# Optimization experiments

Measured on AMD Instinct MI355X. Metric: run time of the kernel, lower is better.

## Reference

```python
import jax, jax.numpy as jnp
import numpy as np

N, E, F_IN, F_HID, F_OUT = 50000, 800000, 128, 128, 64


def setup_inputs() -> dict:
    key = jax.random.key(0)
    k_x, k_e, k_w1, k_w2 = jax.random.split(key, 4)
    x = jax.random.normal(k_x, (N, F_IN), dtype=jnp.float32)
    edge_index = jax.random.randint(k_e, (2, E), 0, N, dtype=jnp.int32)
    # GCNConv params (glorot-ish scale)
    W1 = jax.random.normal(k_w1, (F_IN, F_HID), dtype=jnp.float32) * (1.0 / np.sqrt(F_IN))
    b1 = jnp.zeros((F_HID,), dtype=jnp.float32)
    W2 = jax.random.normal(k_w2, (F_HID, F_OUT), dtype=jnp.float32) * (1.0 / np.sqrt(F_HID))
    b2 = jnp.zeros((F_OUT,), dtype=jnp.float32)
    return {"x": x, "edge_index": edge_index, "W1": W1, "b1": b1, "W2": W2, "b2": b2}


def reference(x, edge_index, W1, b1, W2, b2):
    n = x.shape[0]
    # PyG GCNConv: add self-loops, symmetric normalization deg^-1/2 * deg^-1/2
    loops = jnp.arange(n, dtype=edge_index.dtype)
    src = jnp.concatenate([edge_index[0], loops])  # (E+N,)
    dst = jnp.concatenate([edge_index[1], loops])  # (E+N,)
    deg = jax.ops.segment_sum(jnp.ones_like(dst, dtype=x.dtype), dst, num_segments=n)
    dinv = jnp.where(deg > 0, jax.lax.rsqrt(jnp.maximum(deg, 1.0)), 0.0)
    norm = dinv[src] * dinv[dst]  # (E+N,)

    def conv(h, W, b):
        h = h @ W                               # (n, f_out)
        msg = h[src] * norm[:, None]            # gather + scale, (E+N, f_out)
        return jax.ops.segment_sum(msg, dst, num_segments=n) + b

    h = jax.nn.relu(conv(x, W1, b1))  # dropout p=0.0 -> identity
    return conv(h, W2, b2)
```

## Files before the change

kernel.cpp:

```cpp
#include <hip/hip_runtime.h>

typedef __bf16 bf16x8 __attribute__((ext_vector_type(8)));
typedef float  f32x4  __attribute__((ext_vector_type(4)));
typedef int    i32x4  __attribute__((ext_vector_type(4)));
typedef unsigned int u32x4 __attribute__((ext_vector_type(4)));

#define NTLOAD(p)    __builtin_nontemporal_load(p)

__device__ __forceinline__ float bf2f(unsigned short h) {
    return __uint_as_float(((unsigned int)h) << 16);
}
__device__ __forceinline__ unsigned short f2bf(float f) {
    unsigned int u = __float_as_uint(f);
    u += 0x7FFFu + ((u >> 16) & 1u);
    return (unsigned short)(u >> 16);
}
__device__ __forceinline__ void unpack8(u32x4 u, float* v) {
#pragma unroll
    for (int k = 0; k < 4; ++k) {
        v[2 * k]     = __uint_as_float(u[k] << 16);
        v[2 * k + 1] = __uint_as_float(u[k] & 0xFFFF0000u);
    }
}

__global__ void k1_deg_detect(const int* __restrict__ dst, int* __restrict__ deg,
                              int* __restrict__ rank, int E,
                              const unsigned short* __restrict__ x, int* __restrict__ cnt,
                              int degBlocks) {
    if ((int)blockIdx.x < degBlocks) {
        int e0 = (blockIdx.x * 256 + threadIdx.x) * 8;
        if (e0 + 8 <= E) {
            i32x4 d0 = NTLOAD((i32x4*)(dst + e0));
            i32x4 d1 = NTLOAD((i32x4*)(dst + e0 + 4));
            i32x4 r0, r1;
#pragma unroll
            for (int k = 0; k < 4; ++k) r0[k] = atomicAdd(&deg[d0[k]], 1);
#pragma unroll
            for (int k = 0; k < 4; ++k) r1[k] = atomicAdd(&deg[d1[k]], 1);
            *(i32x4*)(rank + e0)     = r0;
            *(i32x4*)(rank + e0 + 4) = r1;
        } else {
            for (int e = e0; e < E; ++e) rank[e] = atomicAdd(&deg[dst[e]], 1);
        }
    } else {
        int c = 0;
        for (int i = threadIdx.x; i < 4096; i += 256) {
            unsigned e = (x[i] >> 7) & 0xFFu;
            if (e >= 0x88u) ++c;
        }
        if (c) atomicAdd(cnt, c);
    }
}

template <int COLS>
__device__ __forceinline__ void prepack_one(const void* W, unsigned short* Wp, int idx,
                                            bool isf32) {
    if (idx >= (COLS / 16) * 4 * 64) return;
    int lane = idx & 63;
    int ks   = (idx >> 6) & 3;
    int nt   = idx >> 8;
    int col  = nt * 16 + (lane & 15);
    int krow = ks * 32 + (lane >> 4) * 8;
    unsigned short tmp[8];
#pragma unroll
    for (int j = 0; j < 8; ++j) {
        size_t e = (size_t)(krow + j) * COLS + col;
        float v = isf32 ? ((const float*)W)[e] : bf2f(((const unsigned short*)W)[e]);
        tmp[j] = f2bf(v);
    }
    *(u32x4*)(Wp + (size_t)idx * 8) = *(u32x4*)tmp;
}

__global__ void k2_scan1_prep(const int* __restrict__ deg, int* __restrict__ offs,
                              int* __restrict__ bsum, float* __restrict__ dinv, int N, int NB,
                              const void* __restrict__ W1, const void* __restrict__ W2,
                              const void* __restrict__ b1, const void* __restrict__ b2,
                              unsigned short* __restrict__ Wp1, unsigned short* __restrict__ Wp2,
                              float* __restrict__ b1f, float* __restrict__ b2f,
                              const int* __restrict__ cnt) {
    __shared__ int s[256];
    int t = threadIdx.x;
    if ((int)blockIdx.x < NB) {
        int base = blockIdx.x * 1024 + t * 4;
        int d4[4];
#pragma unroll
        for (int k = 0; k < 4; ++k) d4[k] = (base + k < N) ? deg[base + k] : 0;
#pragma unroll
        for (int k = 0; k < 4; ++k)
            if (base + k < N) dinv[base + k] = rsqrtf((float)d4[k] + 1.0f);
        int mySum = d4[0] + d4[1] + d4[2] + d4[3];
        s[t] = mySum;
        __syncthreads();
        for (int d = 1; d < 256; d <<= 1) {
            int v = (t >= d) ? s[t - d] : 0;
            __syncthreads();
            s[t] += v;
            __syncthreads();
        }
        int run = s[t] - mySum;
#pragma unroll
        for (int k = 0; k < 4; ++k) {
            if (base + k < N) offs[base + k] = run;
            run += d4[k];
        }
        if (t == 255) bsum[blockIdx.x] = s[255];
    } else {
        bool isf32 = (*cnt >= 16);
        int bid = blockIdx.x - NB;
        if (bid < 8) {
            prepack_one<128>(W1, Wp1, bid * 256 + t, isf32);
        } else if (bid < 12) {
            prepack_one<64>(W2, Wp2, (bid - 8) * 256 + t, isf32);
        } else {
            if (t < 128) b1f[t] = isf32 ? ((const float*)b1)[t]
                                        : bf2f(((const unsigned short*)b1)[t]);
            else if (t < 192) b2f[t - 128] = isf32 ? ((const float*)b2)[t - 128]
                                                   : bf2f(((const unsigned short*)b2)[t - 128]);
        }
    }
}

__global__ void scan23(const int* __restrict__ bsum, int* __restrict__ offs,
                       int N, int E, int NB) {
    __shared__ int s[256];
    int t = threadIdx.x;
    s[t] = (t < NB) ? bsum[t] : 0;
    __syncthreads();
    for (int d = 1; d < 256; d <<= 1) {
        int v = (t >= d) ? s[t - d] : 0;
        __syncthreads();
        s[t] += v;
        __syncthreads();
    }
    int boff = (blockIdx.x > 0) ? s[blockIdx.x - 1] : 0;
    int base = blockIdx.x * 1024 + t * 4;
#pragma unroll
    for (int k = 0; k < 4; ++k) {
        int i = base + k;
        if (i < N) offs[i] += boff;
    }
    if (blockIdx.x == 0 && t == 0) offs[N] = E;
}

__device__ __forceinline__ void gemm1_body(const void* __restrict__ X,
                                           const unsigned short* __restrict__ Wp,
                                           const float* __restrict__ dinv,
                                           unsigned short* __restrict__ O, int nstrips,
                                           bool xf32, int blockI) {
    constexpr int NT = 8;
    const int wave = threadIdx.x >> 6;
    const int lane = threadIdx.x & 63;
    const int strip = blockI * 4 + wave;
    if (strip >= nstrips) return;
    const int m = lane & 15;
    const int q = lane >> 4;
    const unsigned rowoff = (unsigned)(strip * 16 + m) * 128u + (unsigned)(q * 8);

    f32x4 acc[NT];
#pragma unroll
    for (int nt = 0; nt < NT; ++nt) acc[nt] = (f32x4){0.f, 0.f, 0.f, 0.f};

#pragma unroll
    for (int ks = 0; ks < 4; ++ks) {
        bf16x8 a;
        if (xf32) {
            const float* xp = (const float*)X + rowoff + ks * 32;
            f32x4 u = NTLOAD((f32x4*)xp);
            f32x4 v = NTLOAD((f32x4*)xp + 1);
            unsigned short tmp[8];
            tmp[0] = f2bf(u[0]); tmp[1] = f2bf(u[1]); tmp[2] = f2bf(u[2]); tmp[3] = f2bf(u[3]);
            tmp[4] = f2bf(v[0]); tmp[5] = f2bf(v[1]); tmp[6] = f2bf(v[2]); tmp[7] = f2bf(v[3]);
            a = *(bf16x8*)tmp;
        } else {
            a = NTLOAD((bf16x8*)((const unsigned short*)X + rowoff + ks * 32));
        }
#pragma unroll
        for (int nt = 0; nt < NT; ++nt) {
            bf16x8 b = *(const bf16x8*)(Wp + (unsigned)(((nt * 4 + ks) * 64 + lane) * 8));
            acc[nt] = __builtin_amdgcn_mfma_f32_16x16x32_bf16(a, b, acc[nt], 0, 0, 0);
        }
    }

    const int r0 = strip * 16 + q * 4;
    f32x4 dv = *(const f32x4*)(dinv + r0);
    float dr[4] = {dv[0], dv[1], dv[2], dv[3]};
#pragma unroll
    for (int nt = 0; nt < NT; ++nt) {
#pragma unroll
        for (int r = 0; r < 4; ++r)
            O[(unsigned)(r0 + r) * 128u + (unsigned)(nt * 16 + m)] = f2bf(acc[nt][r] * dr[r]);
    }
}

__global__ __launch_bounds__(256) void k5_scatter_gemm1(
        const int* __restrict__ src, const int* __restrict__ dst,
        const int* __restrict__ offs, const int* __restrict__ rank,
        int* __restrict__ adj, int E, int SB,
        const void* __restrict__ X, const unsigned short* __restrict__ Wp,
        const float* __restrict__ dinv,
        unsigned short* __restrict__ O, int nstrips, const int* __restrict__ cnt) {
    if ((int)blockIdx.x < SB) {
        int e0 = (blockIdx.x * 256 + threadIdx.x) * 8;
        if (e0 + 8 <= E) {
            i32x4 d0 = NTLOAD((i32x4*)(dst + e0));
            i32x4 d1 = NTLOAD((i32x4*)(dst + e0 + 4));
            i32x4 s0 = NTLOAD((i32x4*)(src + e0));
            i32x4 s1 = NTLOAD((i32x4*)(src + e0 + 4));
            i32x4 r0 = NTLOAD((i32x4*)(rank + e0));
            i32x4 r1 = NTLOAD((i32x4*)(rank + e0 + 4));
            adj[offs[d0[0]] + r0[0]] = s0[0];
            adj[offs[d0[1]] + r0[1]] = s0[1];
            adj[offs[d0[2]] + r0[2]] = s0[2];
            adj[offs[d0[3]] + r0[3]] = s0[3];
            adj[offs[d1[0]] + r1[0]] = s1[0];
            adj[offs[d1[1]] + r1[1]] = s1[1];
            adj[offs[d1[2]] + r1[2]] = s1[2];
            adj[offs[d1[3]] + r1[3]] = s1[3];
        } else {
            for (int e = e0; e < E; ++e) adj[offs[dst[e]] + rank[e]] = src[e];
        }
    } else {
        gemm1_body(X, Wp, dinv, O, nstrips, (*cnt >= 16), blockIdx.x - SB);
    }
}

__global__ __launch_bounds__(256) void gather1_gemm2(
        const unsigned short* __restrict__ Hb, const float* __restrict__ dinv,
        const float* __restrict__ b, const int* __restrict__ offs,
        const int* __restrict__ adj, const unsigned short* __restrict__ Wp2,
        unsigned short* __restrict__ H2b, int N) {
    __shared__ unsigned short Rs[16][136];
    const int strip = blockIdx.x;
    const int lane = threadIdx.x & 63;

    {
        int ndl = threadIdx.x >> 4;
        int nd = strip * 16 + ndl;
        int l15 = lane & 15;
        int gbase = lane & ~15;
        unsigned f8 = (unsigned)(l15 * 8);
        if (nd < N) {
            float acc[8];
#pragma unroll
            for (int k = 0; k < 8; ++k) acc[k] = 0.f;
            int beg = offs[nd], end = offs[nd + 1];
            for (int c = beg; c < end; c += 16) {
                int rem = end - c;
                int myadj = (l15 < rem) ? NTLOAD((int*)&adj[c + l15]) : 0;
#pragma unroll
                for (int t = 0; t < 16; t += 8) {
                    if (t >= rem) break;
                    int sI[8];
#pragma unroll
                    for (int k = 0; k < 8; ++k) sI[k] = __shfl(myadj, gbase + t + k, 64);
                    u32x4 u[8];
#pragma unroll
                    for (int k = 0; k < 8; ++k)
                        u[k] = *(const u32x4*)(Hb + ((unsigned)sI[k] << 7) + f8);
                    float n[8];
#pragma unroll
                    for (int k = 0; k < 8; ++k) n[k] = (t + k < rem) ? 1.f : 0.f;
#pragma unroll
                    for (int k = 0; k < 8; ++k) {
                        float v[8];
                        unpack8(u[k], v);
#pragma unroll
                        for (int j = 0; j < 8; ++j) acc[j] = fmaf(v[j], n[k], acc[j]);
                    }
                }
            }
            float dd = dinv[nd];
            float hv[8], bb[8];
            unpack8(*(const u32x4*)(Hb + ((unsigned)nd << 7) + f8), hv);
            *(f32x4*)&bb[0] = *(const f32x4*)(b + f8);
            *(f32x4*)&bb[4] = *(const f32x4*)(b + f8 + 4);
            unsigned short o[8];
#pragma unroll
            for (int k = 0; k < 8; ++k) {
                float a = fmaf(acc[k] + hv[k], dd, bb[k]);
                o[k] = f2bf(fmaxf(a, 0.f));
            }
            *(u32x4*)&Rs[ndl][f8] = *(u32x4*)o;
        } else {
            *(u32x4*)&Rs[ndl][f8] = (u32x4){0u, 0u, 0u, 0u};
        }
    }
    __syncthreads();

    {
        const int nt = threadIdx.x >> 6;
        const int m = lane & 15;
        const int q = lane >> 4;
        f32x4 acc = (f32x4){0.f, 0.f, 0.f, 0.f};
#pragma unroll
        for (int ks = 0; ks < 4; ++ks) {
            bf16x8 a = *(const bf16x8*)&Rs[m][ks * 32 + q * 8];
            bf16x8 bfr = *(const bf16x8*)(Wp2 + (unsigned)(((nt * 4 + ks) * 64 + lane) * 8));
            acc = __builtin_amdgcn_mfma_f32_16x16x32_bf16(a, bfr, acc, 0, 0, 0);
        }
        const int r0 = strip * 16 + q * 4;
        if (r0 + 3 < N) {
            f32x4 dv = *(const f32x4*)(dinv + r0);
#pragma unroll
            for (int r = 0; r < 4; ++r)
                H2b[(unsigned)(r0 + r) * 64u + (unsigned)(nt * 16 + m)] = f2bf(acc[r] * dv[r]);
        } else {
#pragma unroll
            for (int r = 0; r < 4; ++r) {
                int row = r0 + r;
                if (row < N)
                    H2b[(unsigned)row * 64u + (unsigned)(nt * 16 + m)] =
                        f2bf(acc[r] * dinv[row]);
            }
        }
    }
}

__global__ void gather2(const unsigned short* __restrict__ H2b, const float* __restrict__ dinv,
                        const float* __restrict__ b, const int* __restrict__ offs,
                        const int* __restrict__ adj, void* __restrict__ out,
                        int N, const int* __restrict__ cnt) {
    bool isf32 = (*cnt >= 16);
    int nd = blockIdx.x * 32 + (threadIdx.x >> 3);
    int lane = threadIdx.x & 63;
    int l7 = lane & 7;
    int gbase = lane & ~7;
    unsigned f8 = (unsigned)(l7 * 8);
    if (nd >= N) return;

    float acc[8];
#pragma unroll
    for (int k = 0; k < 8; ++k) acc[k] = 0.f;

    int beg = offs[nd], end = offs[nd + 1];
    for (int c = beg; c < end; c += 8) {
        int rem = end - c;
        int myadj = (l7 < rem) ? NTLOAD((int*)&adj[c + l7]) : 0;
        int sI[8];
#pragma unroll
        for (int k = 0; k < 8; ++k) sI[k] = __shfl(myadj, gbase + k, 64);
        u32x4 u[8];
#pragma unroll
        for (int k = 0; k < 8; ++k)
            u[k] = *(const u32x4*)(H2b + ((unsigned)sI[k] << 6) + f8);
        float n[8];
#pragma unroll
        for (int k = 0; k < 8; ++k) n[k] = (k < rem) ? 1.f : 0.f;
#pragma unroll
        for (int k = 0; k < 8; ++k) {
            float v[8];
            unpack8(u[k], v);
#pragma unroll
            for (int j = 0; j < 8; ++j) acc[j] = fmaf(v[j], n[k], acc[j]);
        }
    }
    float dd = dinv[nd];
    float hv[8], bb[8];
    unpack8(*(const u32x4*)(H2b + ((unsigned)nd << 6) + f8), hv);
    *(f32x4*)&bb[0] = *(const f32x4*)(b + f8);
    *(f32x4*)&bb[4] = *(const f32x4*)(b + f8 + 4);
    float r[8];
#pragma unroll
    for (int k = 0; k < 8; ++k) r[k] = fmaf(acc[k] + hv[k], dd, bb[k]);
    if (isf32) {
        float* op = (float*)out + (unsigned)nd * 64u + f8;
        *(f32x4*)op       = *(f32x4*)&r[0];
        *(f32x4*)(op + 4) = *(f32x4*)&r[4];
    } else {
        unsigned short o[8];
#pragma unroll
        for (int k = 0; k < 8; ++k) o[k] = f2bf(r[k]);
        *(u32x4*)((unsigned short*)out + (unsigned)nd * 64u + f8) = *(u32x4*)o;
    }
}

extern "C" void kernel_launch(void* const* d_in, const int* in_sizes, int n_in,
                              void* d_out, int out_size, void* d_ws, size_t ws_size,
                              hipStream_t stream) {
    const void* x  = d_in[0];
    const int*  ei = (const int*)d_in[1];
    const void* W1 = d_in[2];
    const void* b1 = d_in[3];
    const void* W2 = d_in[4];
    const void* b2 = d_in[5];

    const int N = in_sizes[0] / 128;
    const int E = in_sizes[1] / 2;
    const int* src = ei;
    const int* dst = ei + E;

    float* ws = (float*)d_ws;
    size_t off = 0;
    auto alloc = [&](size_t n) { size_t p = off; off += (n + 15) & ~(size_t)15; return p; };
    int*   cnt    = (int*)(ws + alloc(64));
    int*   deg    = (int*)(ws + alloc(N));
    float* dinv   = ws + alloc(N);
    int*   offs   = (int*)(ws + alloc(N + 1));
    int*   bsum   = (int*)(ws + alloc(256));
    int*   adj    = (int*)(ws + alloc(E));
    int*   rank   = (int*)(ws + alloc(E));
    unsigned short* Hb  = (unsigned short*)(ws + alloc((size_t)N * 64));
    unsigned short* Wp1 = (unsigned short*)(ws + alloc(8192));
    unsigned short* Wp2 = (unsigned short*)(ws + alloc(4096));
    float* b1f    = ws + alloc(128);
    float* b2f    = ws + alloc(64);
    unsigned short* H2b = (unsigned short*)(ws + alloc((size_t)N * 32));

    hipMemsetAsync(ws, 0, (64 + ((size_t)(N + 15) & ~(size_t)15)) * sizeof(float), stream);

    const int EB8 = (E + 2047) / 2048;
    const int NB = (N + 1023) / 1024;
    const int nstrips = (N + 15) / 16;
    const int GB = (nstrips + 3) / 4;

    k1_deg_detect<<<EB8 + 1, 256, 0, stream>>>(dst, deg, rank, E,
                                               (const unsigned short*)x, cnt, EB8);
    k2_scan1_prep<<<NB + 13, 256, 0, stream>>>(deg, offs, bsum, dinv, N, NB,
                                               W1, W2, b1, b2, Wp1, Wp2, b1f, b2f, cnt);
    scan23<<<NB, 256, 0, stream>>>(bsum, offs, N, E, NB);
    k5_scatter_gemm1<<<EB8 + GB, 256, 0, stream>>>(src, dst, offs, rank, adj, E, EB8,
                                                   x, Wp1, dinv, Hb, nstrips, cnt);
    gather1_gemm2<<<nstrips, 256, 0, stream>>>(Hb, dinv, b1f, offs, adj, Wp2, H2b, N);
    gather2<<<(N + 31) / 32, 256, 0, stream>>>(H2b, dinv, b2f, offs, adj, d_out, N, cnt);
}
```

Before: 191.2 us.

## Double-buffer neighbor gathers and double threads per node in both gather kernels

Both gather kernels now assign twice as many threads per destination node, each loading 8-byte slices instead of 16-byte slices. The neighbor loop is software-pipelined with two register buffers, so the next 8 neighbor rows are issued before the current 8 are accumulated. Adjacency indices are fetched in 32-wide windows and refreshed as needed. The aim is more memory-level parallelism and better latency hiding on the random row gathers. The cost is more threads and narrower loads, and gather1_gemm2 now uses 512-thread blocks with half the threads idle during the MFMA phase.

```diff
diff --git a/kernel.cpp b/kernel.cpp
--- a/kernel.cpp
+++ b/kernel.cpp
@@ -14,13 +14,6 @@
     unsigned int u = __float_as_uint(f);
     u += 0x7FFFu + ((u >> 16) & 1u);
     return (unsigned short)(u >> 16);
-}
-__device__ __forceinline__ void unpack8(u32x4 u, float* v) {
-#pragma unroll
-    for (int k = 0; k < 4; ++k) {
-        v[2 * k]     = __uint_as_float(u[k] << 16);
-        v[2 * k + 1] = __uint_as_float(u[k] & 0xFFFF0000u);
-    }
 }
 
 __global__ void k1_deg_detect(const int* __restrict__ dst, int* __restrict__ deg,
@@ -224,71 +217,94 @@
     }
 }
 
-__global__ __launch_bounds__(256) void gather1_gemm2(
+__global__ __launch_bounds__(512) void gather1_gemm2(
         const unsigned short* __restrict__ Hb, const float* __restrict__ dinv,
         const float* __restrict__ b, const int* __restrict__ offs,
         const int* __restrict__ adj, const unsigned short* __restrict__ Wp2,
         unsigned short* __restrict__ H2b, int N) {
     __shared__ unsigned short Rs[16][136];
     const int strip = blockIdx.x;
-    const int lane = threadIdx.x & 63;
+    const int tid = threadIdx.x;
+    const int lane = tid & 63;
 
     {
-        int ndl = threadIdx.x >> 4;
+        int ndl = tid >> 5;
         int nd = strip * 16 + ndl;
-        int l15 = lane & 15;
-        int gbase = lane & ~15;
-        unsigned f8 = (unsigned)(l15 * 8);
+        int l31 = tid & 31;
+        int gbase = lane & ~31;
+        unsigned fb = (unsigned)(l31 * 4);
         if (nd < N) {
-            float acc[8];
-#pragma unroll
-            for (int k = 0; k < 8; ++k) acc[k] = 0.f;
             int beg = offs[nd], end = offs[nd + 1];
-            for (int c = beg; c < end; c += 16) {
-                int rem = end - c;
-                int myadj = (l15 < rem) ? NTLOAD((int*)&adj[c + l15]) : 0;
-#pragma unroll
-                for (int t = 0; t < 16; t += 8) {
-                    if (t >= rem) break;
-                    int sI[8];
-#pragma unroll
-                    for (int k = 0; k < 8; ++k) sI[k] = __shfl(myadj, gbase + t + k, 64);
-                    u32x4 u[8];
-#pragma unroll
-                    for (int k = 0; k < 8; ++k)
-                        u[k] = *(const u32x4*)(Hb + ((unsigned)sI[k] << 7) + f8);
-                    float n[8];
-#pragma unroll
-                    for (int k = 0; k < 8; ++k) n[k] = (t + k < rem) ? 1.f : 0.f;
-#pragma unroll
-                    for (int k = 0; k < 8; ++k) {
-                        float v[8];
-                        unpack8(u[k], v);
-#pragma unroll
-                        for (int j = 0; j < 8; ++j) acc[j] = fmaf(v[j], n[k], acc[j]);
-                    }
+            int wbase = beg;
+            int ma = (wbase + l31 < end) ? adj[wbase + l31] : 0;
+            uint2 self = *(const uint2*)(Hb + ((unsigned)nd << 7) + fb);
+            float dd = dinv[nd];
+            f32x4 bb = *(const f32x4*)(b + fb);
+
+            float acc[4] = {0.f, 0.f, 0.f, 0.f};
+            uint2 ua[8], ub[8];
+
+            auto issue8 = [&](uint2* u, int c0) {
+                int off = c0 - wbase;
+#pragma unroll
+                for (int k = 0; k < 8; ++k) {
+                    int s = __shfl(ma, gbase + off + k, 64);
+                    u[k] = *(const uint2*)(Hb + ((unsigned)s << 7) + fb);
                 }
+            };
+            auto consume8 = [&](const uint2* u, int c0) {
+#pragma unroll
+                for (int k = 0; k < 8; ++k) {
+                    float w = (c0 + k < end) ? 1.f : 0.f;
+                    acc[0] = fmaf(__uint_as_float(u[k].x << 16), w, acc[0]);
+                    acc[1] = fmaf(__uint_as_float(u[k].x & 0xFFFF0000u), w, acc[1]);
+                    acc[2] = fmaf(__uint_as_float(u[k].y << 16), w, acc[2]);
+                    acc[3] = fmaf(__uint_as_float(u[k].y & 0xFFFF0000u), w, acc[3]);
+                }
+            };
+            auto refresh = [&](int c0) {
+                if (c0 - wbase >= 32) {
+                    wbase = c0;
+                    ma = (wbase + l31 < end) ? adj[wbase + l31] : 0;
+                }
+            };
+
+            int cA = beg;
+            issue8(ua, cA);
+            for (;;) {
+                int cB = cA + 8;
+                if (cB < end) {
+                    refresh(cB);
+                    issue8(ub, cB);
+                    consume8(ua, cA);
+                    int cN = cB + 8;
+                    if (cN < end) {
+                        refresh(cN);
+                        issue8(ua, cN);
+                        consume8(ub, cB);
+                        cA = cN;
+                    } else { consume8(ub, cB); break; }
+                } else { consume8(ua, cA); break; }
             }
-            float dd = dinv[nd];
-            float hv[8], bb[8];
-            unpack8(*(const u32x4*)(Hb + ((unsigned)nd << 7) + f8), hv);
-            *(f32x4*)&bb[0] = *(const f32x4*)(b + f8);
-            *(f32x4*)&bb[4] = *(const f32x4*)(b + f8 + 4);
-            unsigned short o[8];
-#pragma unroll
-            for (int k = 0; k < 8; ++k) {
-                float a = fmaf(acc[k] + hv[k], dd, bb[k]);
-                o[k] = f2bf(fmaxf(a, 0.f));
-            }
-            *(u32x4*)&Rs[ndl][f8] = *(u32x4*)o;
-        } else {
-            *(u32x4*)&Rs[ndl][f8] = (u32x4){0u, 0u, 0u, 0u};
+
+            float s0 = __uint_as_float(self.x << 16);
+            float s1 = __uint_as_float(self.x & 0xFFFF0000u);
+            float s2 = __uint_as_float(self.y << 16);
+            float s3 = __uint_as_float(self.y & 0xFFFF0000u);
+            unsigned short o[4];
+            o[0] = f2bf(fmaxf(fmaf(acc[0] + s0, dd, bb[0]), 0.f));
+            o[1] = f2bf(fmaxf(fmaf(acc[1] + s1, dd, bb[1]), 0.f));
+            o[2] = f2bf(fmaxf(fmaf(acc[2] + s2, dd, bb[2]), 0.f));
+            o[3] = f2bf(fmaxf(fmaf(acc[3] + s3, dd, bb[3]), 0.f));
+            *(uint2*)&Rs[ndl][fb] = *(uint2*)o;
+        } else {
+            *(uint2*)&Rs[ndl][(unsigned)((tid & 31) * 4)] = make_uint2(0u, 0u);
         }
     }
     __syncthreads();
 
-    {
-        const int nt = threadIdx.x >> 6;
+    if (tid < 256) {
+        const int nt = tid >> 6;
         const int m = lane & 15;
         const int q = lane >> 4;
         f32x4 acc = (f32x4){0.f, 0.f, 0.f, 0.f};
@@ -316,61 +332,92 @@
     }
 }
 
-__global__ void gather2(const unsigned short* __restrict__ H2b, const float* __restrict__ dinv,
-                        const float* __restrict__ b, const int* __restrict__ offs,
-                        const int* __restrict__ adj, void* __restrict__ out,
-                        int N, const int* __restrict__ cnt) {
+__global__ __launch_bounds__(256) void gather2(
+        const unsigned short* __restrict__ H2b, const float* __restrict__ dinv,
+        const float* __restrict__ b, const int* __restrict__ offs,
+        const int* __restrict__ adj, void* __restrict__ out,
+        int N, const int* __restrict__ cnt) {
     bool isf32 = (*cnt >= 16);
-    int nd = blockIdx.x * 32 + (threadIdx.x >> 3);
-    int lane = threadIdx.x & 63;
-    int l7 = lane & 7;
-    int gbase = lane & ~7;
-    unsigned f8 = (unsigned)(l7 * 8);
+    const int tid = threadIdx.x;
+    int nd = blockIdx.x * 16 + (tid >> 4);
+    int lane = tid & 63;
+    int l15 = tid & 15;
+    int gbase = lane & ~15;
+    unsigned fb = (unsigned)(l15 * 4);
     if (nd >= N) return;
 
-    float acc[8];
-#pragma unroll
-    for (int k = 0; k < 8; ++k) acc[k] = 0.f;
-
     int beg = offs[nd], end = offs[nd + 1];
-    for (int c = beg; c < end; c += 8) {
-        int rem = end - c;
-        int myadj = (l7 < rem) ? NTLOAD((int*)&adj[c + l7]) : 0;
-        int sI[8];
-#pragma unroll
-        for (int k = 0; k < 8; ++k) sI[k] = __shfl(myadj, gbase + k, 64);
-        u32x4 u[8];
-#pragma unroll
-        for (int k = 0; k < 8; ++k)
-            u[k] = *(const u32x4*)(H2b + ((unsigned)sI[k] << 6) + f8);
-        float n[8];
-#pragma unroll
-        for (int k = 0; k < 8; ++k) n[k] = (k < rem) ? 1.f : 0.f;
+    int wbase = beg;
+    int ma0 = (wbase + l15 < end)      ? adj[wbase + l15]      : 0;
+    int ma1 = (wbase + 16 + l15 < end) ? adj[wbase + 16 + l15] : 0;
+    uint2 self = *(const uint2*)(H2b + ((unsigned)nd << 6) + fb);
+    float dd = dinv[nd];
+    f32x4 bb = *(const f32x4*)(b + fb);
+
+    float acc[4] = {0.f, 0.f, 0.f, 0.f};
+    uint2 ua[8], ub[8];
+
+    auto issue8 = [&](uint2* u, int c0) {
+        int off = c0 - wbase;
+        int mam = (off & 16) ? ma1 : ma0;
+        int lsel = gbase + (off & 8);
 #pragma unroll
         for (int k = 0; k < 8; ++k) {
-            float v[8];
-            unpack8(u[k], v);
-#pragma unroll
-            for (int j = 0; j < 8; ++j) acc[j] = fmaf(v[j], n[k], acc[j]);
-        }
-    }
-    float dd = dinv[nd];
-    float hv[8], bb[8];
-    unpack8(*(const u32x4*)(H2b + ((unsigned)nd << 6) + f8), hv);
-    *(f32x4*)&bb[0] = *(const f32x4*)(b + f8);
-    *(f32x4*)&bb[4] = *(const f32x4*)(b + f8 + 4);
-    float r[8];
-#pragma unroll
-    for (int k = 0; k < 8; ++k) r[k] = fmaf(acc[k] + hv[k], dd, bb[k]);
+            int s = __shfl(mam, lsel + k, 64);
+            u[k] = *(const uint2*)(H2b + ((unsigned)s << 6) + fb);
+        }
+    };
+    auto consume8 = [&](const uint2* u, int c0) {
+#pragma unroll
+        for (int k = 0; k < 8; ++k) {
+            float w = (c0 + k < end) ? 1.f : 0.f;
+            acc[0] = fmaf(__uint_as_float(u[k].x << 16), w, acc[0]);
+            acc[1] = fmaf(__uint_as_float(u[k].x & 0xFFFF0000u), w, acc[1]);
+            acc[2] = fmaf(__uint_as_float(u[k].y << 16), w, acc[2]);
+            acc[3] = fmaf(__uint_as_float(u[k].y & 0xFFFF0000u), w, acc[3]);
+        }
+    };
+    auto refresh = [&](int c0) {
+        if (c0 - wbase >= 32) {
+            wbase = c0;
+            ma0 = (wbase + l15 < end)      ? adj[wbase + l15]      : 0;
+            ma1 = (wbase + 16 + l15 < end) ? adj[wbase + 16 + l15] : 0;
+        }
+    };
+
+    int cA = beg;
+    issue8(ua, cA);
+    for (;;) {
+        int cB = cA + 8;
+        if (cB < end) {
+            refresh(cB);
+            issue8(ub, cB);
+            consume8(ua, cA);
+            int cN = cB + 8;
+            if (cN < end) {
+                refresh(cN);
+                issue8(ua, cN);
+                consume8(ub, cB);
+                cA = cN;
+            } else { consume8(ub, cB); break; }
+        } else { consume8(ua, cA); break; }
+    }
+
+    float s0 = __uint_as_float(self.x << 16);
+    float s1 = __uint_as_float(self.x & 0xFFFF0000u);
+    float s2 = __uint_as_float(self.y << 16);
+    float s3 = __uint_as_float(self.y & 0xFFFF0000u);
+    float r0 = fmaf(acc[0] + s0, dd, bb[0]);
+    float r1 = fmaf(acc[1] + s1, dd, bb[1]);
+    float r2 = fmaf(acc[2] + s2, dd, bb[2]);
+    float r3 = fmaf(acc[3] + s3, dd, bb[3]);
     if (isf32) {
-        float* op = (float*)out + (unsigned)nd * 64u + f8;
-        *(f32x4*)op       = *(f32x4*)&r[0];
-        *(f32x4*)(op + 4) = *(f32x4*)&r[4];
+        float* op = (float*)out + (unsigned)nd * 64u + fb;
+        *(f32x4*)op = (f32x4){r0, r1, r2, r3};
     } else {
-        unsigned short o[8];
-#pragma unroll
-        for (int k = 0; k < 8; ++k) o[k] = f2bf(r[k]);
-        *(u32x4*)((unsigned short*)out + (unsigned)nd * 64u + f8) = *(u32x4*)o;
+        unsigned short o[4];
+        o[0] = f2bf(r0); o[1] = f2bf(r1); o[2] = f2bf(r2); o[3] = f2bf(r3);
+        *(uint2*)((unsigned short*)out + (unsigned)nd * 64u + fb) = *(uint2*)o;
     }
 }
 
@@ -420,6 +467,6 @@
     scan23<<<NB, 256, 0, stream>>>(bsum, offs, N, E, NB);
     k5_scatter_gemm1<<<EB8 + GB, 256, 0, stream>>>(src, dst, offs, rank, adj, E, EB8,
                                                    x, Wp1, dinv, Hb, nstrips, cnt);
-    gather1_gemm2<<<nstrips, 256, 0, stream>>>(Hb, dinv, b1f, offs, adj, Wp2, H2b, N);
-    gather2<<<(N + 31) / 32, 256, 0, stream>>>(H2b, dinv, b2f, offs, adj, d_out, N, cnt);
-}
+    gather1_gemm2<<<nstrips, 512, 0, stream>>>(Hb, dinv, b1f, offs, adj, Wp2, H2b, N);
+    gather2<<<(N + 15) / 16, 256, 0, stream>>>(H2b, dinv, b2f, offs, adj, d_out, N, cnt);
+}
```

After: 201.0 us. +5.2%, slower.

## Split layer-1 gather into two feature-half passes to shrink gathered working set

Applied to the files above, without the earlier changes.

The layer-1 aggregation is split into two kernels, each gathering one 64-feature half (128 bytes per row) of Hb, so the randomly accessed working set per pass is half the size and fits better in cache. The first pass writes its relu'd half to a new buffer R1a; the second gathers the other half, combines both in shared memory, and runs the GEMM2 MFMA on 32-row tiles. The adjacency and offsets are now read twice and there is an extra launch plus an intermediate write and read. It also drops nontemporal hints on the GEMM1 x loads and aligns the Hb/H2b buffers to 256 bytes.

```diff
diff --git a/kernel.cpp b/kernel.cpp
--- a/kernel.cpp
+++ b/kernel.cpp
@@ -165,14 +165,14 @@
         bf16x8 a;
         if (xf32) {
             const float* xp = (const float*)X + rowoff + ks * 32;
-            f32x4 u = NTLOAD((f32x4*)xp);
-            f32x4 v = NTLOAD((f32x4*)xp + 1);
+            f32x4 u = *(const f32x4*)xp;
+            f32x4 v = *((const f32x4*)xp + 1);
             unsigned short tmp[8];
             tmp[0] = f2bf(u[0]); tmp[1] = f2bf(u[1]); tmp[2] = f2bf(u[2]); tmp[3] = f2bf(u[3]);
             tmp[4] = f2bf(v[0]); tmp[5] = f2bf(v[1]); tmp[6] = f2bf(v[2]); tmp[7] = f2bf(v[3]);
             a = *(bf16x8*)tmp;
         } else {
-            a = NTLOAD((bf16x8*)((const unsigned short*)X + rowoff + ks * 32));
+            a = *(const bf16x8*)((const unsigned short*)X + rowoff + ks * 32);
         }
 #pragma unroll
         for (int nt = 0; nt < NT; ++nt) {
@@ -224,93 +224,149 @@
     }
 }
 
-__global__ __launch_bounds__(256) void gather1_gemm2(
+__global__ __launch_bounds__(256) void gather1_half0(
         const unsigned short* __restrict__ Hb, const float* __restrict__ dinv,
         const float* __restrict__ b, const int* __restrict__ offs,
-        const int* __restrict__ adj, const unsigned short* __restrict__ Wp2,
-        unsigned short* __restrict__ H2b, int N) {
-    __shared__ unsigned short Rs[16][136];
-    const int strip = blockIdx.x;
-    const int lane = threadIdx.x & 63;
+        const int* __restrict__ adj, unsigned short* __restrict__ R1a, int N) {
+    int nd = blockIdx.x * 32 + (threadIdx.x >> 3);
+    int lane = threadIdx.x & 63;
+    int l7 = threadIdx.x & 7;
+    int gbase = lane & ~7;
+    unsigned f8 = (unsigned)(l7 * 8);
+    if (nd >= N) return;
+
+    float acc[8];
+#pragma unroll
+    for (int k = 0; k < 8; ++k) acc[k] = 0.f;
+
+    int beg = offs[nd], end = offs[nd + 1];
+    for (int c = beg; c < end; c += 8) {
+        int rem = end - c;
+        int myadj = (l7 < rem) ? NTLOAD((int*)&adj[c + l7]) : 0;
+        int sI[8];
+#pragma unroll
+        for (int k = 0; k < 8; ++k) sI[k] = __shfl(myadj, gbase + k, 64);
+        u32x4 u[8];
+#pragma unroll
+        for (int k = 0; k < 8; ++k)
+            u[k] = *(const u32x4*)(Hb + ((unsigned)sI[k] << 7) + f8);
+        float n[8];
+#pragma unroll
+        for (int k = 0; k < 8; ++k) n[k] = (k < rem) ? 1.f : 0.f;
+#pragma unroll
+        for (int k = 0; k < 8; ++k) {
+            float v[8];
+            unpack8(u[k], v);
+#pragma unroll
+            for (int j = 0; j < 8; ++j) acc[j] = fmaf(v[j], n[k], acc[j]);
+        }
+    }
+    float dd = dinv[nd];
+    float hv[8], bb[8];
+    unpack8(*(const u32x4*)(Hb + ((unsigned)nd << 7) + f8), hv);
+    *(f32x4*)&bb[0] = *(const f32x4*)(b + f8);
+    *(f32x4*)&bb[4] = *(const f32x4*)(b + f8 + 4);
+    unsigned short o[8];
+#pragma unroll
+    for (int k = 0; k < 8; ++k)
+        o[k] = f2bf(fmaxf(fmaf(acc[k] + hv[k], dd, bb[k]), 0.f));
+    *(u32x4*)(R1a + ((unsigned)nd << 6) + f8) = *(u32x4*)o;
+}
+
+__global__ __launch_bounds__(256) void gather1_half1_gemm2(
+        const unsigned short* __restrict__ Hb, const unsigned short* __restrict__ R1a,
+        const float* __restrict__ dinv, const float* __restrict__ b,
+        const int* __restrict__ offs, const int* __restrict__ adj,
+        const unsigned short* __restrict__ Wp2, unsigned short* __restrict__ H2b, int N) {
+    __shared__ unsigned short Rs[32][136];
+    const int tid = threadIdx.x;
+    const int lane = tid & 63;
 
     {
-        int ndl = threadIdx.x >> 4;
-        int nd = strip * 16 + ndl;
-        int l15 = lane & 15;
-        int gbase = lane & ~15;
-        unsigned f8 = (unsigned)(l15 * 8);
+        int ndl = tid >> 3;
+        int nd = blockIdx.x * 32 + ndl;
+        int l7 = tid & 7;
+        int gbase = lane & ~7;
+        unsigned f8 = (unsigned)(l7 * 8);
         if (nd < N) {
+            u32x4 lh = *(const u32x4*)(R1a + ((unsigned)nd << 6) + f8);
             float acc[8];
 #pragma unroll
             for (int k = 0; k < 8; ++k) acc[k] = 0.f;
             int beg = offs[nd], end = offs[nd + 1];
-            for (int c = beg; c < end; c += 16) {
+            for (int c = beg; c < end; c += 8) {
                 int rem = end - c;
-                int myadj = (l15 < rem) ? NTLOAD((int*)&adj[c + l15]) : 0;
-#pragma unroll
-                for (int t = 0; t < 16; t += 8) {
-                    if (t >= rem) break;
-                    int sI[8];
-#pragma unroll
-                    for (int k = 0; k < 8; ++k) sI[k] = __shfl(myadj, gbase + t + k, 64);
-                    u32x4 u[8];
-#pragma unroll
-                    for (int k = 0; k < 8; ++k)
-                        u[k] = *(const u32x4*)(Hb + ((unsigned)sI[k] << 7) + f8);
-                    float n[8];
-#pragma unroll
-                    for (int k = 0; k < 8; ++k) n[k] = (t + k < rem) ? 1.f : 0.f;
-#pragma unroll
-                    for (int k = 0; k < 8; ++k) {
-                        float v[8];
-                        unpack8(u[k], v);
-#pragma unroll
-                        for (int j = 0; j < 8; ++j) acc[j] = fmaf(v[j], n[k], acc[j]);
-                    }
+                int myadj = (l7 < rem) ? NTLOAD((int*)&adj[c + l7]) : 0;
+                int sI[8];
+#pragma unroll
+                for (int k = 0; k < 8; ++k) sI[k] = __shfl(myadj, gbase + k, 64);
+                u32x4 u[8];
+#pragma unroll
+                for (int k = 0; k < 8; ++k)
+                    u[k] = *(const u32x4*)(Hb + ((unsigned)sI[k] << 7) + 64u + f8);
+                float n[8];
+#pragma unroll
+                for (int k = 0; k < 8; ++k) n[k] = (k < rem) ? 1.f : 0.f;
+#pragma unroll
+                for (int k = 0; k < 8; ++k) {
+                    float v[8];
+                    unpack8(u[k], v);
+#pragma unroll
+                    for (int j = 0; j < 8; ++j) acc[j] = fmaf(v[j], n[k], acc[j]);
                 }
             }
             float dd = dinv[nd];
             float hv[8], bb[8];
-            unpack8(*(const u32x4*)(Hb + ((unsigned)nd << 7) + f8), hv);
-            *(f32x4*)&bb[0] = *(const f32x4*)(b + f8);
-            *(f32x4*)&bb[4] = *(const f32x4*)(b + f8 + 4);
+            unpack8(*(const u32x4*)(Hb + ((unsigned)nd << 7) + 64u + f8), hv);
+            *(f32x4*)&bb[0] = *(const f32x4*)(b + 64u + f8);
+            *(f32x4*)&bb[4] = *(const f32x4*)(b + 64u + f8 + 4);
             unsigned short o[8];
 #pragma unroll
-            for (int k = 0; k < 8; ++k) {
-                float a = fmaf(acc[k] + hv[k], dd, bb[k]);
-                o[k] = f2bf(fmaxf(a, 0.f));
-            }
-            *(u32x4*)&Rs[ndl][f8] = *(u32x4*)o;
+            for (int k = 0; k < 8; ++k)
+                o[k] = f2bf(fmaxf(fmaf(acc[k] + hv[k], dd, bb[k]), 0.f));
+            *(u32x4*)&Rs[ndl][64 + f8] = *(u32x4*)o;
+            *(u32x4*)&Rs[ndl][f8] = lh;
         } else {
-            *(u32x4*)&Rs[ndl][f8] = (u32x4){0u, 0u, 0u, 0u};
+            u32x4 z = (u32x4){0u, 0u, 0u, 0u};
+            *(u32x4*)&Rs[ndl][f8] = z;
+            *(u32x4*)&Rs[ndl][64 + f8] = z;
         }
     }
     __syncthreads();
 
     {
-        const int nt = threadIdx.x >> 6;
+        const int nt = tid >> 6;
         const int m = lane & 15;
         const int q = lane >> 4;
-        f32x4 acc = (f32x4){0.f, 0.f, 0.f, 0.f};
+        f32x4 acc0 = (f32x4){0.f, 0.f, 0.f, 0.f};
+        f32x4 acc1 = (f32x4){0.f, 0.f, 0.f, 0.f};
 #pragma unroll
         for (int ks = 0; ks < 4; ++ks) {
-            bf16x8 a = *(const bf16x8*)&Rs[m][ks * 32 + q * 8];
             bf16x8 bfr = *(const bf16x8*)(Wp2 + (unsigned)(((nt * 4 + ks) * 64 + lane) * 8));
-            acc = __builtin_amdgcn_mfma_f32_16x16x32_bf16(a, bfr, acc, 0, 0, 0);
-        }
-        const int r0 = strip * 16 + q * 4;
-        if (r0 + 3 < N) {
-            f32x4 dv = *(const f32x4*)(dinv + r0);
-#pragma unroll
-            for (int r = 0; r < 4; ++r)
-                H2b[(unsigned)(r0 + r) * 64u + (unsigned)(nt * 16 + m)] = f2bf(acc[r] * dv[r]);
-        } else {
-#pragma unroll
-            for (int r = 0; r < 4; ++r) {
-                int row = r0 + r;
-                if (row < N)
-                    H2b[(unsigned)row * 64u + (unsigned)(nt * 16 + m)] =
-                        f2bf(acc[r] * dinv[row]);
+            bf16x8 a0 = *(const bf16x8*)&Rs[m][ks * 32 + q * 8];
+            bf16x8 a1 = *(const bf16x8*)&Rs[16 + m][ks * 32 + q * 8];
+            acc0 = __builtin_amdgcn_mfma_f32_16x16x32_bf16(a0, bfr, acc0, 0, 0, 0);
+            acc1 = __builtin_amdgcn_mfma_f32_16x16x32_bf16(a1, bfr, acc1, 0, 0, 0);
+        }
+        const int base = blockIdx.x * 32;
+#pragma unroll
+        for (int rt = 0; rt < 2; ++rt) {
+            const f32x4& a = rt ? acc1 : acc0;
+            int r0 = base + rt * 16 + q * 4;
+            if (r0 + 3 < N) {
+                f32x4 dv = *(const f32x4*)(dinv + r0);
+#pragma unroll
+                for (int r = 0; r < 4; ++r)
+                    H2b[(unsigned)(r0 + r) * 64u + (unsigned)(nt * 16 + m)] =
+                        f2bf(a[r] * dv[r]);
+            } else {
+#pragma unroll
+                for (int r = 0; r < 4; ++r) {
+                    int row = r0 + r;
+                    if (row < N)
+                        H2b[(unsigned)row * 64u + (unsigned)(nt * 16 + m)] =
+                            f2bf(a[r] * dinv[row]);
+                }
             }
         }
     }
@@ -392,6 +448,10 @@
     float* ws = (float*)d_ws;
     size_t off = 0;
     auto alloc = [&](size_t n) { size_t p = off; off += (n + 15) & ~(size_t)15; return p; };
+    auto alloc256 = [&](size_t n) {
+        off = (off + 63) & ~(size_t)63;
+        size_t p = off; off += (n + 63) & ~(size_t)63; return p;
+    };
     int*   cnt    = (int*)(ws + alloc(64));
     int*   deg    = (int*)(ws + alloc(N));
     float* dinv   = ws + alloc(N);
@@ -399,12 +459,13 @@
     int*   bsum   = (int*)(ws + alloc(256));
     int*   adj    = (int*)(ws + alloc(E));
     int*   rank   = (int*)(ws + alloc(E));
-    unsigned short* Hb  = (unsigned short*)(ws + alloc((size_t)N * 64));
+    unsigned short* Hb  = (unsigned short*)(ws + alloc256((size_t)N * 64));
     unsigned short* Wp1 = (unsigned short*)(ws + alloc(8192));
     unsigned short* Wp2 = (unsigned short*)(ws + alloc(4096));
     float* b1f    = ws + alloc(128);
     float* b2f    = ws + alloc(64);
-    unsigned short* H2b = (unsigned short*)(ws + alloc((size_t)N * 32));
+    unsigned short* H2b = (unsigned short*)(ws + alloc256((size_t)N * 32));
+    unsigned short* R1a = (unsigned short*)(ws + alloc256((size_t)N * 32));
 
     hipMemsetAsync(ws, 0, (64 + ((size_t)(N + 15) & ~(size_t)15)) * sizeof(float), stream);
 
@@ -412,6 +473,7 @@
     const int NB = (N + 1023) / 1024;
     const int nstrips = (N + 15) / 16;
     const int GB = (nstrips + 3) / 4;
+    const int NB32 = (N + 31) / 32;
 
     k1_deg_detect<<<EB8 + 1, 256, 0, stream>>>(dst, deg, rank, E,
                                                (const unsigned short*)x, cnt, EB8);
@@ -420,6 +482,8 @@
     scan23<<<NB, 256, 0, stream>>>(bsum, offs, N, E, NB);
     k5_scatter_gemm1<<<EB8 + GB, 256, 0, stream>>>(src, dst, offs, rank, adj, E, EB8,
                                                    x, Wp1, dinv, Hb, nstrips, cnt);
-    gather1_gemm2<<<nstrips, 256, 0, stream>>>(Hb, dinv, b1f, offs, adj, Wp2, H2b, N);
-    gather2<<<(N + 31) / 32, 256, 0, stream>>>(H2b, dinv, b2f, offs, adj, d_out, N, cnt);
-}
+    gather1_half0<<<NB32, 256, 0, stream>>>(Hb, dinv, b1f, offs, adj, R1a, N);
+    gather1_half1_gemm2<<<NB32, 256, 0, stream>>>(Hb, R1a, dinv, b1f, offs, adj,
+                                                  Wp2, H2b, N);
+    gather2<<<NB32, 256, 0, stream>>>(H2b, dinv, b2f, offs, adj, d_out, N, cnt);
+}
```

After: 198.0 us. 3.6% more time.

## Overlap layer-1 GEMM with degree counting and build CSR via atomic cursors

Applied to the files above, without the earlier changes.

Restructures the pipeline so the first GEMM no longer depends on dinv: it runs in the same launch as degree counting, and the source-side normalization is applied per edge during the gather instead. The rank array is replaced by a per-node position cursor that is advanced atomically during the scatter, and the memset is replaced by a prep kernel that zeroes deg and packs the weights. This removes the dependency that serialized GEMM1 behind the scan and drops the rank write/read traffic. In exchange it adds an extra launch, a dinv gather and shuffle per edge in the gather, and scatter atomics that make adjacency order nondeterministic.

```diff
diff --git a/kernel.cpp b/kernel.cpp
--- a/kernel.cpp
+++ b/kernel.cpp
@@ -20,35 +20,6 @@
     for (int k = 0; k < 4; ++k) {
         v[2 * k]     = __uint_as_float(u[k] << 16);
         v[2 * k + 1] = __uint_as_float(u[k] & 0xFFFF0000u);
-    }
-}
-
-__global__ void k1_deg_detect(const int* __restrict__ dst, int* __restrict__ deg,
-                              int* __restrict__ rank, int E,
-                              const unsigned short* __restrict__ x, int* __restrict__ cnt,
-                              int degBlocks) {
-    if ((int)blockIdx.x < degBlocks) {
-        int e0 = (blockIdx.x * 256 + threadIdx.x) * 8;
-        if (e0 + 8 <= E) {
-            i32x4 d0 = NTLOAD((i32x4*)(dst + e0));
-            i32x4 d1 = NTLOAD((i32x4*)(dst + e0 + 4));
-            i32x4 r0, r1;
-#pragma unroll
-            for (int k = 0; k < 4; ++k) r0[k] = atomicAdd(&deg[d0[k]], 1);
-#pragma unroll
-            for (int k = 0; k < 4; ++k) r1[k] = atomicAdd(&deg[d1[k]], 1);
-            *(i32x4*)(rank + e0)     = r0;
-            *(i32x4*)(rank + e0 + 4) = r1;
-        } else {
-            for (int e = e0; e < E; ++e) rank[e] = atomicAdd(&deg[dst[e]], 1);
-        }
-    } else {
-        int c = 0;
-        for (int i = threadIdx.x; i < 4096; i += 256) {
-            unsigned e = (x[i] >> 7) & 0xFFu;
-            if (e >= 0x88u) ++c;
-        }
-        if (c) atomicAdd(cnt, c);
     }
 }
 
@@ -71,80 +42,43 @@
     *(u32x4*)(Wp + (size_t)idx * 8) = *(u32x4*)tmp;
 }
 
-__global__ void k2_scan1_prep(const int* __restrict__ deg, int* __restrict__ offs,
-                              int* __restrict__ bsum, float* __restrict__ dinv, int N, int NB,
-                              const void* __restrict__ W1, const void* __restrict__ W2,
-                              const void* __restrict__ b1, const void* __restrict__ b2,
-                              unsigned short* __restrict__ Wp1, unsigned short* __restrict__ Wp2,
-                              float* __restrict__ b1f, float* __restrict__ b2f,
-                              const int* __restrict__ cnt) {
-    __shared__ int s[256];
+__global__ void k0_prep(const unsigned short* __restrict__ x, int* __restrict__ cnt,
+                        int* __restrict__ deg, int N,
+                        const void* __restrict__ W1, const void* __restrict__ W2,
+                        const void* __restrict__ b1, const void* __restrict__ b2,
+                        unsigned short* __restrict__ Wp1, unsigned short* __restrict__ Wp2,
+                        float* __restrict__ b1f, float* __restrict__ b2f) {
     int t = threadIdx.x;
-    if ((int)blockIdx.x < NB) {
-        int base = blockIdx.x * 1024 + t * 4;
-        int d4[4];
-#pragma unroll
-        for (int k = 0; k < 4; ++k) d4[k] = (base + k < N) ? deg[base + k] : 0;
-#pragma unroll
-        for (int k = 0; k < 4; ++k)
-            if (base + k < N) dinv[base + k] = rsqrtf((float)d4[k] + 1.0f);
-        int mySum = d4[0] + d4[1] + d4[2] + d4[3];
-        s[t] = mySum;
+    if (blockIdx.x == 0) {
+        __shared__ int sc[256];
+        int c = 0;
+        for (int i = t; i < 4096; i += 256) {
+            unsigned e = (x[i] >> 7) & 0xFFu;
+            if (e >= 0x88u) ++c;
+        }
+        sc[t] = c;
         __syncthreads();
-        for (int d = 1; d < 256; d <<= 1) {
-            int v = (t >= d) ? s[t - d] : 0;
+        for (int d = 128; d > 0; d >>= 1) {
+            if (t < d) sc[t] += sc[t + d];
             __syncthreads();
-            s[t] += v;
-            __syncthreads();
-        }
-        int run = s[t] - mySum;
-#pragma unroll
-        for (int k = 0; k < 4; ++k) {
-            if (base + k < N) offs[base + k] = run;
-            run += d4[k];
-        }
-        if (t == 255) bsum[blockIdx.x] = s[255];
+        }
+        bool isf32 = (sc[0] >= 16);
+        if (t == 0) cnt[0] = sc[0];
+        for (int i = t; i < 2048; i += 256) prepack_one<128>(W1, Wp1, i, isf32);
+        for (int i = t; i < 1024; i += 256) prepack_one<64>(W2, Wp2, i, isf32);
+        if (t < 128) b1f[t] = isf32 ? ((const float*)b1)[t]
+                                    : bf2f(((const unsigned short*)b1)[t]);
+        else if (t < 192) b2f[t - 128] = isf32 ? ((const float*)b2)[t - 128]
+                                               : bf2f(((const unsigned short*)b2)[t - 128]);
     } else {
-        bool isf32 = (*cnt >= 16);
-        int bid = blockIdx.x - NB;
-        if (bid < 8) {
-            prepack_one<128>(W1, Wp1, bid * 256 + t, isf32);
-        } else if (bid < 12) {
-            prepack_one<64>(W2, Wp2, (bid - 8) * 256 + t, isf32);
-        } else {
-            if (t < 128) b1f[t] = isf32 ? ((const float*)b1)[t]
-                                        : bf2f(((const unsigned short*)b1)[t]);
-            else if (t < 192) b2f[t - 128] = isf32 ? ((const float*)b2)[t - 128]
-                                                   : bf2f(((const unsigned short*)b2)[t - 128]);
-        }
-    }
-}
-
-__global__ void scan23(const int* __restrict__ bsum, int* __restrict__ offs,
-                       int N, int E, int NB) {
-    __shared__ int s[256];
-    int t = threadIdx.x;
-    s[t] = (t < NB) ? bsum[t] : 0;
-    __syncthreads();
-    for (int d = 1; d < 256; d <<= 1) {
-        int v = (t >= d) ? s[t - d] : 0;
-        __syncthreads();
-        s[t] += v;
-        __syncthreads();
-    }
-    int boff = (blockIdx.x > 0) ? s[blockIdx.x - 1] : 0;
-    int base = blockIdx.x * 1024 + t * 4;
-#pragma unroll
-    for (int k = 0; k < 4; ++k) {
-        int i = base + k;
-        if (i < N) offs[i] += boff;
-    }
-    if (blockIdx.x == 0 && t == 0) offs[N] = E;
+        int i = ((int)blockIdx.x - 1) * 1024 + t * 4;
+        if (i + 4 <= N) *(i32x4*)(deg + i) = (i32x4){0, 0, 0, 0};
+        else for (int k = i; k < N; ++k) deg[k] = 0;
+    }
 }
 
 __device__ __forceinline__ void gemm1_body(const void* __restrict__ X,
                                            const unsigned short* __restrict__ Wp,
-                                           const float* __restrict__ dinv,
                                            unsigned short* __restrict__ O, int nstrips,
                                            bool xf32, int blockI) {
     constexpr int NT = 8;
@@ -165,14 +99,14 @@
         bf16x8 a;
         if (xf32) {
             const float* xp = (const float*)X + rowoff + ks * 32;
-            f32x4 u = NTLOAD((f32x4*)xp);
-            f32x4 v = NTLOAD((f32x4*)xp + 1);
+            f32x4 u = *(const f32x4*)xp;
+            f32x4 v = *((const f32x4*)xp + 1);
             unsigned short tmp[8];
             tmp[0] = f2bf(u[0]); tmp[1] = f2bf(u[1]); tmp[2] = f2bf(u[2]); tmp[3] = f2bf(u[3]);
             tmp[4] = f2bf(v[0]); tmp[5] = f2bf(v[1]); tmp[6] = f2bf(v[2]); tmp[7] = f2bf(v[3]);
             a = *(bf16x8*)tmp;
         } else {
-            a = NTLOAD((bf16x8*)((const unsigned short*)X + rowoff + ks * 32));
+            a = *(const bf16x8*)((const unsigned short*)X + rowoff + ks * 32);
         }
 #pragma unroll
         for (int nt = 0; nt < NT; ++nt) {
@@ -182,45 +116,104 @@
     }
 
     const int r0 = strip * 16 + q * 4;
-    f32x4 dv = *(const f32x4*)(dinv + r0);
-    float dr[4] = {dv[0], dv[1], dv[2], dv[3]};
 #pragma unroll
     for (int nt = 0; nt < NT; ++nt) {
 #pragma unroll
         for (int r = 0; r < 4; ++r)
-            O[(unsigned)(r0 + r) * 128u + (unsigned)(nt * 16 + m)] = f2bf(acc[nt][r] * dr[r]);
-    }
-}
-
-__global__ __launch_bounds__(256) void k5_scatter_gemm1(
-        const int* __restrict__ src, const int* __restrict__ dst,
-        const int* __restrict__ offs, const int* __restrict__ rank,
-        int* __restrict__ adj, int E, int SB,
-        const void* __restrict__ X, const unsigned short* __restrict__ Wp,
-        const float* __restrict__ dinv,
-        unsigned short* __restrict__ O, int nstrips, const int* __restrict__ cnt) {
-    if ((int)blockIdx.x < SB) {
+            O[(unsigned)(r0 + r) * 128u + (unsigned)(nt * 16 + m)] = f2bf(acc[nt][r]);
+    }
+}
+
+__global__ __launch_bounds__(256) void k1_deg_gemm1(
+        const int* __restrict__ dst, int* __restrict__ deg, int E, int DB,
+        const void* __restrict__ X, const unsigned short* __restrict__ Wp1,
+        unsigned short* __restrict__ Hb, int nstrips, const int* __restrict__ cnt) {
+    if ((int)blockIdx.x < DB) {
         int e0 = (blockIdx.x * 256 + threadIdx.x) * 8;
         if (e0 + 8 <= E) {
             i32x4 d0 = NTLOAD((i32x4*)(dst + e0));
             i32x4 d1 = NTLOAD((i32x4*)(dst + e0 + 4));
-            i32x4 s0 = NTLOAD((i32x4*)(src + e0));
-            i32x4 s1 = NTLOAD((i32x4*)(src + e0 + 4));
-            i32x4 r0 = NTLOAD((i32x4*)(rank + e0));
-            i32x4 r1 = NTLOAD((i32x4*)(rank + e0 + 4));
-            adj[offs[d0[0]] + r0[0]] = s0[0];
-            adj[offs[d0[1]] + r0[1]] = s0[1];
-            adj[offs[d0[2]] + r0[2]] = s0[2];
-            adj[offs[d0[3]] + r0[3]] = s0[3];
-            adj[offs[d1[0]] + r1[0]] = s1[0];
-            adj[offs[d1[1]] + r1[1]] = s1[1];
-            adj[offs[d1[2]] + r1[2]] = s1[2];
-            adj[offs[d1[3]] + r1[3]] = s1[3];
+#pragma unroll
+            for (int k = 0; k < 4; ++k) atomicAdd(&deg[d0[k]], 1);
+#pragma unroll
+            for (int k = 0; k < 4; ++k) atomicAdd(&deg[d1[k]], 1);
         } else {
-            for (int e = e0; e < E; ++e) adj[offs[dst[e]] + rank[e]] = src[e];
+            for (int e = e0; e < E; ++e) atomicAdd(&deg[dst[e]], 1);
         }
     } else {
-        gemm1_body(X, Wp, dinv, O, nstrips, (*cnt >= 16), blockIdx.x - SB);
+        gemm1_body(X, Wp1, Hb, nstrips, (*cnt >= 16), blockIdx.x - DB);
+    }
+}
+
+__global__ void k2_scan1(const int* __restrict__ deg, int* __restrict__ offs,
+                         int* __restrict__ bsum, float* __restrict__ dinv, int N) {
+    __shared__ int s[256];
+    int t = threadIdx.x;
+    int base = blockIdx.x * 1024 + t * 4;
+    int d4[4];
+#pragma unroll
+    for (int k = 0; k < 4; ++k) d4[k] = (base + k < N) ? deg[base + k] : 0;
+#pragma unroll
+    for (int k = 0; k < 4; ++k)
+        if (base + k < N) dinv[base + k] = rsqrtf((float)d4[k] + 1.0f);
+    int mySum = d4[0] + d4[1] + d4[2] + d4[3];
+    s[t] = mySum;
+    __syncthreads();
+    for (int d = 1; d < 256; d <<= 1) {
+        int v = (t >= d) ? s[t - d] : 0;
+        __syncthreads();
+        s[t] += v;
+        __syncthreads();
+    }
+    int run = s[t] - mySum;
+#pragma unroll
+    for (int k = 0; k < 4; ++k) {
+        if (base + k < N) offs[base + k] = run;
+        run += d4[k];
+    }
+    if (t == 255) bsum[blockIdx.x] = s[255];
+}
+
+__global__ void scan23(const int* __restrict__ bsum, int* __restrict__ offs,
+                       int* __restrict__ pos, int N, int E, int NB) {
+    __shared__ int s[256];
+    int t = threadIdx.x;
+    s[t] = (t < NB) ? bsum[t] : 0;
+    __syncthreads();
+    for (int d = 1; d < 256; d <<= 1) {
+        int v = (t >= d) ? s[t - d] : 0;
+        __syncthreads();
+        s[t] += v;
+        __syncthreads();
+    }
+    int boff = (blockIdx.x > 0) ? s[blockIdx.x - 1] : 0;
+    int base = blockIdx.x * 1024 + t * 4;
+#pragma unroll
+    for (int k = 0; k < 4; ++k) {
+        int i = base + k;
+        if (i < N) {
+            int v = offs[i] + boff;
+            offs[i] = v;
+            pos[i] = v;
+        }
+    }
+    if (blockIdx.x == 0 && t == 0) offs[N] = E;
+}
+
+__global__ void k4_scatter(const int* __restrict__ src, const int* __restrict__ dst,
+                           int* __restrict__ pos, int* __restrict__ adj, int E) {
+    int e0 = (blockIdx.x * 256 + threadIdx.x) * 8;
+    if (e0 + 8 <= E) {
+        i32x4 d0 = NTLOAD((i32x4*)(dst + e0));
+        i32x4 d1 = NTLOAD((i32x4*)(dst + e0 + 4));
+        i32x4 s0 = NTLOAD((i32x4*)(src + e0));
+        i32x4 s1 = NTLOAD((i32x4*)(src + e0 + 4));
+#pragma unroll
+        for (int k = 0; k < 4; ++k) adj[atomicAdd(&pos[d0[k]], 1)] = s0[k];
+#pragma unroll
+        for (int k = 0; k < 4; ++k) adj[atomicAdd(&pos[d1[k]], 1)] = s1[k];
+    } else {
+        for (int e = e0; e < E; ++e) adj[atomicAdd(&pos[dst[e]], 1)] = src[e];
     }
 }
 
@@ -231,10 +224,11 @@
         unsigned short* __restrict__ H2b, int N) {
     __shared__ unsigned short Rs[16][136];
     const int strip = blockIdx.x;
-    const int lane = threadIdx.x & 63;
+    const int tid = threadIdx.x;
+    const int lane = tid & 63;
 
     {
-        int ndl = threadIdx.x >> 4;
+        int ndl = tid >> 4;
         int nd = strip * 16 + ndl;
         int l15 = lane & 15;
         int gbase = lane & ~15;
@@ -247,6 +241,7 @@
             for (int c = beg; c < end; c += 16) {
                 int rem = end - c;
                 int myadj = (l15 < rem) ? NTLOAD((int*)&adj[c + l15]) : 0;
+                float myw = (l15 < rem) ? dinv[myadj] : 0.f;
 #pragma unroll
                 for (int t = 0; t < 16; t += 8) {
                     if (t >= rem) break;
@@ -259,7 +254,7 @@
                         u[k] = *(const u32x4*)(Hb + ((unsigned)sI[k] << 7) + f8);
                     float n[8];
 #pragma unroll
-                    for (int k = 0; k < 8; ++k) n[k] = (t + k < rem) ? 1.f : 0.f;
+                    for (int k = 0; k < 8; ++k) n[k] = __shfl(myw, gbase + t + k, 64);
 #pragma unroll
                     for (int k = 0; k < 8; ++k) {
                         float v[8];
@@ -277,18 +272,18 @@
             unsigned short o[8];
 #pragma unroll
             for (int k = 0; k < 8; ++k) {
-                float a = fmaf(acc[k] + hv[k], dd, bb[k]);
+                float a = fmaf(fmaf(hv[k], dd, acc[k]), dd, bb[k]);
                 o[k] = f2bf(fmaxf(a, 0.f));
             }
             *(u32x4*)&Rs[ndl][f8] = *(u32x4*)o;
         } else {
-            *(u32x4*)&Rs[ndl][f8] = (u32x4){0u, 0u, 0u, 0u};
+            *(u32x4*)&Rs[ndl][(unsigned)((lane & 15) * 8)] = (u32x4){0u, 0u, 0u, 0u};
         }
     }
     __syncthreads();
 
     {
-        const int nt = threadIdx.x >> 6;
+        const int nt = tid >> 6;
         const int m = lane & 15;
         const int q = lane >> 4;
         f32x4 acc = (f32x4){0.f, 0.f, 0.f, 0.f};
@@ -396,9 +391,9 @@
     int*   deg    = (int*)(ws + alloc(N));
     float* dinv   = ws + alloc(N);
     int*   offs   = (int*)(ws + alloc(N + 1));
+    int*   pos    = (int*)(ws + alloc(N));
     int*   bsum   = (int*)(ws + alloc(256));
     int*   adj    = (int*)(ws + alloc(E));
-    int*   rank   = (int*)(ws + alloc(E));
     unsigned short* Hb  = (unsigned short*)(ws + alloc((size_t)N * 64));
     unsigned short* Wp1 = (unsigned short*)(ws + alloc(8192));
     unsigned short* Wp2 = (unsigned short*)(ws + alloc(4096));
@@ -406,20 +401,20 @@
     float* b2f    = ws + alloc(64);
     unsigned short* H2b = (unsigned short*)(ws + alloc((size_t)N * 32));
 
-    hipMemsetAsync(ws, 0, (64 + ((size_t)(N + 15) & ~(size_t)15)) * sizeof(float), stream);
-
     const int EB8 = (E + 2047) / 2048;
     const int NB = (N + 1023) / 1024;
+    const int DB0 = (N + 1023) / 1024;
     const int nstrips = (N + 15) / 16;
     const int GB = (nstrips + 3) / 4;
-
-    k1_deg_detect<<<EB8 + 1, 256, 0, stream>>>(dst, deg, rank, E,
-                                               (const unsigned short*)x, cnt, EB8);
-    k2_scan1_prep<<<NB + 13, 256, 0, stream>>>(deg, offs, bsum, dinv, N, NB,
-                                               W1, W2, b1, b2, Wp1, Wp2, b1f, b2f, cnt);
-    scan23<<<NB, 256, 0, stream>>>(bsum, offs, N, E, NB);
-    k5_scatter_gemm1<<<EB8 + GB, 256, 0, stream>>>(src, dst, offs, rank, adj, E, EB8,
-                                                   x, Wp1, dinv, Hb, nstrips, cnt);
+    const int NB32 = (N + 31) / 32;
+
+    k0_prep<<<1 + DB0, 256, 0, stream>>>((const unsigned short*)x, cnt, deg, N,
+                                         W1, W2, b1, b2, Wp1, Wp2, b1f, b2f);
+    k1_deg_gemm1<<<EB8 + GB, 256, 0, stream>>>(dst, deg, E, EB8,
+                                               x, Wp1, Hb, nstrips, cnt);
+    k2_scan1<<<NB, 256, 0, stream>>>(deg, offs, bsum, dinv, N);
+    scan23<<<NB, 256, 0, stream>>>(bsum, offs, pos, N, E, NB);
+    k4_scatter<<<EB8, 256, 0, stream>>>(src, dst, pos, adj, E);
     gather1_gemm2<<<nstrips, 256, 0, stream>>>(Hb, dinv, b1f, offs, adj, Wp2, H2b, N);
-    gather2<<<(N + 31) / 32, 256, 0, stream>>>(H2b, dinv, b2f, offs, adj, d_out, N, cnt);
-}
+    gather2<<<NB32, 256, 0, stream>>>(H2b, dinv, b2f, offs, adj, d_out, N, cnt);
+}
```

Result: slower. 239.6 us (+25.3%).
